# Optimization experiments

Measured on AMD Instinct MI355X. Metric: run time of the kernel, lower is better.

## Reference

```python
import jax, jax.numpy as jnp
import numpy as np

VOCAB = 128
NUM_PATHS = 100     # num_paths sampled from the lattice
NBEST_SCALE = 0.5   # scale on scores before sampling (k2.random_paths)
TEMPERATURE = 1.0   # logprob temperature before normalization
BLANK = 0           # CTC blank token


def setup_inputs() -> dict:
    key = jax.random.key(0)
    k1, k2, k3, k4 = jax.random.split(key, 4)
    B, T, L = 8, 500, 100
    logits = jax.random.normal(k1, (B, T, VOCAB), jnp.float32)
    emissions = jax.nn.log_softmax(logits, -1)  # acoustic-model log-probs (N, T, C)
    emissions_lengths = jax.random.randint(k2, (B,), 400, T + 1).astype(jnp.int32)
    labels = jax.random.randint(k3, (B, L), 1, VOCAB).astype(jnp.int32)
    labels_length = jax.random.randint(k4, (B,), 80, L + 1).astype(jnp.int32)
    return {"emissions": emissions, "emissions_lengths": emissions_lengths,
            "labels": labels, "labels_length": labels_length}


def _mwer(emissions, emissions_lengths, labels, labels_length):
    B, T, V = emissions.shape
    L = labels.shape[1]
    P = NUM_PATHS
    key = jax.random.key(1)
    # --- N-best path sampling: Gumbel perturbation of nbest_scale-scaled log-probs ---
    u = jax.random.uniform(key, (B, P, T, V), emissions.dtype, 1e-6, 1.0 - 1e-6)
    g = -jnp.log(-jnp.log(u))
    tokens = jnp.argmax(emissions[:, None] * NBEST_SCALE + g, axis=-1)  # (B, P, T)
    frame_mask = jnp.arange(T)[None, None, :] < emissions_lengths[:, None, None]
    # path log-prob under the model (unscaled scores), temperature-scaled
    lp = jnp.take_along_axis(emissions[:, None], tokens[..., None], axis=-1)[..., 0]
    path_logp = jnp.sum(jnp.where(frame_mask, lp, 0.0), axis=-1) / TEMPERATURE  # (B, P)
    # --- CTC collapse (ctc_topo semantics: drop blanks + repeats) into padded hyps ---
    prev = jnp.concatenate([jnp.full_like(tokens[..., :1], -1), tokens[..., :-1]], -1)
    keep = (tokens != BLANK) & (tokens != prev) & frame_mask
    pos = jnp.where(keep, jnp.cumsum(keep, -1) - 1, T)  # dropped frames -> dump slot T
    BP = B * P
    tok2, pos2 = tokens.reshape(BP, T), pos.reshape(BP, T)
    hyp = jnp.full((BP, T + 1), -1, tokens.dtype).at[jnp.arange(BP)[:, None], pos2].set(tok2)[:, :T]
    hyp_len = keep.reshape(BP, T).sum(-1)
    # --- Levenshtein alignment: exact edit distance hyp vs ref (vectorized DP) ---
    refs = jnp.repeat(labels, P, axis=0)             # (BP, L)  hyp_to_ref_map
    ref_len = jnp.repeat(labels_length, P, axis=0)   # (BP,)
    dp0 = jnp.broadcast_to(jnp.arange(L + 1, dtype=jnp.int32), (BP, L + 1))
    js = jnp.arange(L + 1, dtype=jnp.int32)[None, :]

    def step(dp, x):
        h, valid = x  # hyp token (BP,), valid flag (BP,)
        cost = (refs != h[:, None]).astype(jnp.int32)                       # (BP, L)
        cand = jnp.concatenate([dp[:, :1] + 1,
                                jnp.minimum(dp[:, 1:] + 1, dp[:, :-1] + cost)], 1)
        # insertion chain new[j] = min(cand[j], new[j-1]+1) via min-plus prefix
        new = jax.lax.cummin(cand - js, axis=1) + js
        return jnp.where(valid[:, None], new, dp), None

    valid = jnp.arange(T)[:, None] < hyp_len[None, :]  # (T, BP)
    dp, _ = jax.lax.scan(step, dp0, (hyp.T, valid))
    wers = jnp.take_along_axis(dp, ref_len[:, None], 1)[:, 0].reshape(B, P)
    wers = jax.lax.stop_gradient(wers.astype(emissions.dtype))
    # --- MWER: normalize path posteriors per utterance, expected WER, 'mean' ---
    prob = jax.nn.softmax(path_logp, axis=1)
    return jnp.mean(prob * wers)


def reference(emissions, emissions_lengths, labels, labels_length):
    return _mwer(emissions, emissions_lengths, labels, labels_length)
```

## Files before the change

kernel.cpp:

```cpp
#include <hip/hip_runtime.h>
#include <stdint.h>

#define NB 8
#define NP 100
#define NT 500
#define NV 128
#define NBP 800
#define TS 512
#define ES 500
#define PAIRS (NB * NT * 25)
#define NSB 1563

typedef unsigned long long u64;

#define ROTL(x, r) __builtin_amdgcn_alignbit((x), (x), 32 - (r))

#define SIDX(v) ((v) + ((v) >> 5))

__device__ __forceinline__ void threefry4_lo(uint32_t cA, uint32_t cB,
                                             uint32_t cC, uint32_t cD,
                                             uint32_t& oA, uint32_t& oB,
                                             uint32_t& oC, uint32_t& oD) {
  const uint32_t K2 = 0x1BD11BDBu;
  uint32_t a0 = 0u, a1 = cA + 1u;
  uint32_t b0 = 0u, b1 = cB + 1u;
  uint32_t c0 = 0u, c1 = cC + 1u;
  uint32_t d0 = 0u, d1 = cD + 1u;
#define PIN4() asm volatile("" : "+v"(a1), "+v"(b1), "+v"(c1), "+v"(d1))
#define R4(r) \
  a0 += a1; b0 += b1; c0 += c1; d0 += d1; \
  a1 = ROTL(a1, r) ^ a0; b1 = ROTL(b1, r) ^ b0; \
  c1 = ROTL(c1, r) ^ c0; d1 = ROTL(d1, r) ^ d0; \
  PIN4();
#define K4(kx, ky) \
  a0 += (kx); b0 += (kx); c0 += (kx); d0 += (kx); \
  a1 += (ky); b1 += (ky); c1 += (ky); d1 += (ky);
  R4(13) R4(15) R4(26) R4(6)
  K4(1u, K2 + 1u)
  R4(17) R4(29) R4(16) R4(24)
  K4(K2, 2u)
  R4(13) R4(15) R4(26) R4(6)
  K4(0u, 4u)
  R4(17) R4(29) R4(16) R4(24)
  K4(1u, K2 + 4u)
  R4(13) R4(15) R4(26) R4(6)
  oA = a1 + 5u; oB = b1 + 5u;
  oC = c1 + 5u; oD = d1 + 5u;
#undef R4
#undef K4
#undef PIN4
}

__global__ __launch_bounds__(256) void k_sample(
    const float* __restrict__ em, const int* __restrict__ elen,
    uint8_t* __restrict__ tok2, float* __restrict__ lp2t,
    const int* __restrict__ labels, const int* __restrict__ llen,
    uint4* __restrict__ pqg) {
  const int tid = threadIdx.x;
  if (blockIdx.x >= NSB) {
    const int b = blockIdx.x - NSB;
    if (tid < NV) {
      const int c = tid;
      const int m = llen[b];
      const int* __restrict__ lab = labels + b * 100;
      uint32_t a0 = 0, a1 = 0, a2 = 0, a3 = 0;
      const int e0 = m < 32 ? m : 32, e1 = m < 64 ? m : 64;
      const int e2 = m < 96 ? m : 96, e3 = m;
      for (int i = 0; i < e0; i++)  a0 |= (uint32_t)(lab[i] == c) << i;
      for (int i = 32; i < e1; i++) a1 |= (uint32_t)(lab[i] == c) << (i - 32);
      for (int i = 64; i < e2; i++) a2 |= (uint32_t)(lab[i] == c) << (i - 64);
      for (int i = 96; i < e3; i++) a3 |= (uint32_t)(lab[i] == c) << (i - 96);
      pqg[b * NV + c] = make_uint4(a0, a1, a2, a3);
    }
    return;
  }
  __shared__ float snw[4][NV + 4];
  const int pi0 = blockIdx.x * 64;
  const int R0 = pi0 / 25;
  for (int i = tid; i < 4 * NV; i += 256) {
    const int r = i >> 7, v = i & 127;
    int R = R0 + r; R = R < NB * NT ? R : NB * NT - 1;
    snw[r][SIDX(v)] = -__builtin_amdgcn_exp2f(em[(size_t)R * NV + v] * -0.7213475204444817f);
  }
  __syncthreads();
  const int gg = blockIdx.x * 256 + tid;
  const int pitem = gg >> 2, q = gg & 3;
  if (pitem >= PAIRS) return;
  const int R = pitem / 25;
  const int pp = pitem - R * 25;
  const int b = R / NT;
  const int t = R - b * NT;
  if (t >= elen[b]) return;
  const int r = R - R0;
  const int vh = q << 5;
  const int sbase = vh + q;
  const int bp0 = b * NP + 4 * pp;
  const uint32_t baseA = ((uint32_t)(bp0 * NT + t) << 7) + (uint32_t)vh;
  const uint32_t baseB = baseA + (uint32_t)(NT << 7);
  const uint32_t baseC = baseB + (uint32_t)(NT << 7);
  const uint32_t baseD = baseC + (uint32_t)(NT << 7);
  const float span = (float)(1.0 - 1e-6) - 1e-6f;
  float bvA = 3.0e38f, bvB = 3.0e38f, bvC = 3.0e38f, bvD = 3.0e38f;
  int biA = 0, biB = 0, biC = 0, biD = 0;
#pragma unroll 8
  for (int i = 0; i < 32; i++) {
    uint32_t rA, rB, rC, rD;
    threefry4_lo(baseA + (uint32_t)i, baseB + (uint32_t)i,
                 baseC + (uint32_t)i, baseD + (uint32_t)i, rA, rB, rC, rD);
    const float w = snw[r][sbase + i];
    const float fA = __uint_as_float((rA >> 9) | 0x3f800000u) - 1.0f;
    const float fB = __uint_as_float((rB >> 9) | 0x3f800000u) - 1.0f;
    const float fC = __uint_as_float((rC >> 9) | 0x3f800000u) - 1.0f;
    const float fD = __uint_as_float((rD >> 9) | 0x3f800000u) - 1.0f;
    const float uA = fmaf(fA, span, 1e-6f);
    const float uB = fmaf(fB, span, 1e-6f);
    const float uC = fmaf(fC, span, 1e-6f);
    const float uD = fmaf(fD, span, 1e-6f);
    const float sA = __log2f(uA) * w;
    const float sB = __log2f(uB) * w;
    const float sC = __log2f(uC) * w;
    const float sD = __log2f(uD) * w;
    if (sA < bvA) { bvA = sA; biA = vh + i; }
    if (sB < bvB) { bvB = sB; biB = vh + i; }
    if (sC < bvC) { bvC = sC; biC = vh + i; }
    if (sD < bvD) { bvD = sD; biD = vh + i; }
  }
#pragma unroll
  for (int off = 1; off <= 2; off <<= 1) {
    float ov; int oi;
    ov = __shfl_xor(bvA, off); oi = __shfl_xor(biA, off);
    if (ov < bvA || (ov == bvA && oi < biA)) { bvA = ov; biA = oi; }
    ov = __shfl_xor(bvB, off); oi = __shfl_xor(biB, off);
    if (ov < bvB || (ov == bvB && oi < biB)) { bvB = ov; biB = oi; }
    ov = __shfl_xor(bvC, off); oi = __shfl_xor(biC, off);
    if (ov < bvC || (ov == bvC && oi < biC)) { bvC = ov; biC = oi; }
    ov = __shfl_xor(bvD, off); oi = __shfl_xor(biD, off);
    if (ov < bvD || (ov == bvD && oi < biD)) { bvD = ov; biD = oi; }
  }
  if (q == 0) {
    const float* __restrict__ erow = em + (size_t)R * NV;
    const float eA = erow[biA], eB = erow[biB], eC = erow[biC], eD = erow[biD];
    tok2[(size_t)(bp0 + 0) * TS + t] = (uint8_t)biA;
    tok2[(size_t)(bp0 + 1) * TS + t] = (uint8_t)biB;
    tok2[(size_t)(bp0 + 2) * TS + t] = (uint8_t)biC;
    tok2[(size_t)(bp0 + 3) * TS + t] = (uint8_t)biD;
    *(float4*)&lp2t[(size_t)t * NBP + bp0] = make_float4(eA, eB, eC, eD);
  }
}

__global__ __launch_bounds__(64) void k_ce(
    const uint8_t* __restrict__ tok2, const uint4* __restrict__ pqg,
    const int* __restrict__ elen, uint4* __restrict__ eqc,
    int* __restrict__ nkept) {
  __shared__ uint4 pqs[NV];
  const int bp = blockIdx.x;
  const int b = bp / NP;
  const int lane = threadIdx.x;
  pqs[lane] = pqg[b * NV + lane];
  pqs[lane + 64] = pqg[b * NV + lane + 64];
  __syncthreads();
  const int el = elen[b];
  const uint8_t* __restrict__ row = tok2 + (size_t)bp * TS;
  uint4* __restrict__ orow = eqc + (size_t)bp * ES;
  int off = 0;
  for (int t0 = 0; t0 < el; t0 += 64) {
    const int t = t0 + lane;
    const bool inb = (t < el);
    const int c = inb ? row[t] : 0;
    const int cp = (t == 0) ? 255 : (inb ? row[t - 1] : 255);
    const bool kept = inb && (c != 0) && (c != cp);
    const u64 mask = __ballot(kept);
    const int idx = off + (int)__builtin_amdgcn_mbcnt_hi(
        (uint32_t)(mask >> 32),
        __builtin_amdgcn_mbcnt_lo((uint32_t)mask, 0u));
    if (kept) orow[idx] = pqs[c];
    off += (int)__popcll(mask);
  }
  if (lane == 0) nkept[bp] = off;
}

__device__ __forceinline__ void loadg(uint4 (&B)[4], int g, const uint4* __restrict__ rowp) {
#pragma unroll
  for (int i = 0; i < 4; i++) {
    int t = g * 4 + i;
    t = t < ES ? t : ES - 1;
    B[i] = rowp[t];
  }
}

__device__ __forceinline__ void procg(const uint4 (&B)[4], int fbase, int nk,
                                      u64 hmask,
                                      u64& Pv0, u64& Pv1, u64& Mv0, u64& Mv1,
                                      int& score) {
#pragma unroll
  for (int i = 0; i < 4; i++) {
    if (fbase + i >= nk) break;
    const u64 Eq0 = (u64)B[i].x | ((u64)B[i].y << 32);
    const u64 Eq1 = (u64)B[i].z | ((u64)B[i].w << 32);
    const u64 Xv0 = Eq0 | Mv0, Xv1 = Eq1 | Mv1;
    const u64 EP0 = Eq0 & Pv0, EP1 = Eq1 & Pv1;
    const u64 sA = EP0 + Pv0;
    const u64 sB = EP1 + Pv1 + (sA < EP0 ? 1ull : 0ull);
    const u64 Xh0 = (sA ^ Pv0) | Eq0;
    const u64 Xh1 = (sB ^ Pv1) | Eq1;
    const u64 Ph0 = Mv0 | ~(Xh0 | Pv0);
    const u64 Ph1 = Mv1 | ~(Xh1 | Pv1);
    const u64 Mh0 = Pv0 & Xh0, Mh1 = Pv1 & Xh1;
    score += (int)((Ph1 & hmask) != 0) - (int)((Mh1 & hmask) != 0);
    const u64 nPh1 = (Ph1 << 1) | (Ph0 >> 63);
    const u64 nPh0 = (Ph0 << 1) | 1ull;
    const u64 nMh1 = (Mh1 << 1) | (Mh0 >> 63);
    const u64 nMh0 = (Mh0 << 1);
    Pv0 = nMh0 | ~(Xv0 | nPh0);
    Pv1 = nMh1 | ~(Xv1 | nPh1);
    Mv0 = nPh0 & Xv0;
    Mv1 = nPh1 & Xv1;
  }
}

__global__ __launch_bounds__(128) void k_dpred(
    const uint4* __restrict__ eqc, const int* __restrict__ nkept,
    const int* __restrict__ llen, const float* __restrict__ lp2t,
    const int* __restrict__ elen, float* __restrict__ wer,
    double* __restrict__ pred) {
  const int blk = blockIdx.x;
  const int tid = threadIdx.x;
  if (blk >= 16) {
    const int i = blk - 16;
    const int b = i >> 2, k = i & 3;
    const bool active = (tid < NP);
    const int p = active ? tid : NP - 1;
    const int el = elen[b];
    const int t0 = k * 125;
    const int t1 = (t0 + 125 < el) ? t0 + 125 : el;
    const float* __restrict__ col = lp2t + b * NP + p;
    double s = 0.0;
#pragma unroll 8
    for (int t = t0; t < t1; t++) s += (double)col[(size_t)t * NBP];
    if (active) pred[(size_t)(b * NP + p) * 4 + k] = s;
    return;
  }
  if (tid >= 64) return;
  const int b = blk >> 1, h = blk & 1;
  const bool active = (tid < 50);
  const int bp = b * NP + h * 50 + (active ? tid : 49);
  const int m = llen[b];
  const int nk = nkept[bp];
  const uint4* __restrict__ rowp = eqc + (size_t)bp * ES;
  u64 Pv0 = ~0ull, Pv1 = ~0ull, Mv0 = 0ull, Mv1 = 0ull;
  int score = m;
  const u64 hmask = 1ull << ((m - 1) & 63);

  const int ngl = (nk + 3) >> 2;
  int ngmax = ngl;
  for (int off = 1; off < 64; off <<= 1) {
    const int o = __shfl_xor(ngmax, off);
    ngmax = o > ngmax ? o : ngmax;
  }
  uint4 B0[4], B1[4], B2[4], B3[4];
  loadg(B0, 0, rowp); loadg(B1, 1, rowp);
  loadg(B2, 2, rowp); loadg(B3, 3, rowp);
  int g = 0;
  while (g + 4 <= ngmax) {
    procg(B0, (g    ) * 4, nk, hmask, Pv0, Pv1, Mv0, Mv1, score);
    loadg(B0, g + 4, rowp);
    procg(B1, (g + 1) * 4, nk, hmask, Pv0, Pv1, Mv0, Mv1, score);
    loadg(B1, g + 5, rowp);
    procg(B2, (g + 2) * 4, nk, hmask, Pv0, Pv1, Mv0, Mv1, score);
    loadg(B2, g + 6, rowp);
    procg(B3, (g + 3) * 4, nk, hmask, Pv0, Pv1, Mv0, Mv1, score);
    loadg(B3, g + 7, rowp);
    g += 4;
  }
  if (g     < ngmax) procg(B0, (g    ) * 4, nk, hmask, Pv0, Pv1, Mv0, Mv1, score);
  if (g + 1 < ngmax) procg(B1, (g + 1) * 4, nk, hmask, Pv0, Pv1, Mv0, Mv1, score);
  if (g + 2 < ngmax) procg(B2, (g + 2) * 4, nk, hmask, Pv0, Pv1, Mv0, Mv1, score);
  if (active) wer[bp] = (float)score;
}

__global__ __launch_bounds__(512) void k_fin(
    const double* __restrict__ pred, const float* __restrict__ wer,
    float* __restrict__ out) {
  __shared__ float partial[NB];
  const int w = threadIdx.x >> 6, lane = threadIdx.x & 63;
  const int base = w * NP;
  float l0 = -1e30f, l1 = -1e30f;
  if (lane < NP) {
    const double* pr = pred + (size_t)(base + lane) * 4;
    l0 = (float)(pr[0] + pr[1] + pr[2] + pr[3]);
  }
  if (lane + 64 < NP) {
    const double* pr = pred + (size_t)(base + lane + 64) * 4;
    l1 = (float)(pr[0] + pr[1] + pr[2] + pr[3]);
  }
  float mx = fmaxf(l0, l1);
  for (int off = 1; off < 64; off <<= 1) mx = fmaxf(mx, __shfl_xor(mx, off));
  const float e0 = (lane < NP) ? __expf(l0 - mx) : 0.0f;
  const float e1 = (lane + 64 < NP) ? __expf(l1 - mx) : 0.0f;
  const float w0 = (lane < NP) ? wer[base + lane] : 0.0f;
  const float w1 = (lane + 64 < NP) ? wer[base + lane + 64] : 0.0f;
  float s = e0 + e1;
  float a = e0 * w0 + e1 * w1;
  for (int off = 1; off < 64; off <<= 1) {
    s += __shfl_xor(s, off);
    a += __shfl_xor(a, off);
  }
  if (lane == 0) partial[w] = a / s;
  __syncthreads();
  if (threadIdx.x == 0) {
    float tot = 0.0f;
    for (int i = 0; i < NB; i++) tot += partial[i];
    out[0] = tot * (1.0f / (float)NBP);
  }
}

extern "C" void kernel_launch(void* const* d_in, const int* in_sizes, int n_in,
                              void* d_out, int out_size, void* d_ws, size_t ws_size,
                              hipStream_t stream) {
  const float* em     = (const float*)d_in[0];
  const int*   elen   = (const int*)d_in[1];
  const int*   labels = (const int*)d_in[2];
  const int*   llen   = (const int*)d_in[3];
  float* out = (float*)d_out;
  char* ws = (char*)d_ws;
  uint4*   eqc   = (uint4*)ws;
  uint8_t* tok2  = (uint8_t*)(ws + 6400000);
  float*   lp2t  = (float*)(ws + 6809600);
  float*   wer   = (float*)(ws + 8409600);
  double*  pred  = (double*)(ws + 8412800);
  int*     nkept = (int*)(ws + 8438400);
  uint4*   pqg   = (uint4*)(ws + 8441600);

  k_sample<<<dim3(NSB + NB), dim3(256), 0, stream>>>(em, elen, tok2, lp2t,
                                                     labels, llen, pqg);
  k_ce<<<dim3(NBP), dim3(64), 0, stream>>>(tok2, pqg, elen, eqc, nkept);
  k_dpred<<<dim3(48), dim3(128), 0, stream>>>(eqc, nkept, llen, lp2t, elen, wer, pred);
  k_fin<<<dim3(1), dim3(512), 0, stream>>>(pred, wer, out);
}
```

Baseline: 189.3 us.

## Transpose Myers bit-parallel edit distance to iterate over reference labels

```diff
diff --git a/kernel.cpp b/kernel.cpp
--- a/kernel.cpp
+++ b/kernel.cpp
@@ -7,7 +7,6 @@
 #define NV 128
 #define NBP 800
 #define TS 512
-#define ES 500
 #define PAIRS (NB * NT * 25)
 #define NSB 1563
 
@@ -53,28 +52,9 @@
 
 __global__ __launch_bounds__(256) void k_sample(
     const float* __restrict__ em, const int* __restrict__ elen,
-    uint8_t* __restrict__ tok2, float* __restrict__ lp2t,
-    const int* __restrict__ labels, const int* __restrict__ llen,
-    uint4* __restrict__ pqg) {
+    uint8_t* __restrict__ tok2, float* __restrict__ lp2t) {
+  __shared__ float snw[4][NV + 4];
   const int tid = threadIdx.x;
-  if (blockIdx.x >= NSB) {
-    const int b = blockIdx.x - NSB;
-    if (tid < NV) {
-      const int c = tid;
-      const int m = llen[b];
-      const int* __restrict__ lab = labels + b * 100;
-      uint32_t a0 = 0, a1 = 0, a2 = 0, a3 = 0;
-      const int e0 = m < 32 ? m : 32, e1 = m < 64 ? m : 64;
-      const int e2 = m < 96 ? m : 96, e3 = m;
-      for (int i = 0; i < e0; i++)  a0 |= (uint32_t)(lab[i] == c) << i;
-      for (int i = 32; i < e1; i++) a1 |= (uint32_t)(lab[i] == c) << (i - 32);
-      for (int i = 64; i < e2; i++) a2 |= (uint32_t)(lab[i] == c) << (i - 64);
-      for (int i = 96; i < e3; i++) a3 |= (uint32_t)(lab[i] == c) << (i - 96);
-      pqg[b * NV + c] = make_uint4(a0, a1, a2, a3);
-    }
-    return;
-  }
-  __shared__ float snw[4][NV + 4];
   const int pi0 = blockIdx.x * 64;
   const int R0 = pi0 / 25;
   for (int i = tid; i < 4 * NV; i += 256) {
@@ -149,19 +129,14 @@
 }
 
 __global__ __launch_bounds__(64) void k_ce(
-    const uint8_t* __restrict__ tok2, const uint4* __restrict__ pqg,
-    const int* __restrict__ elen, uint4* __restrict__ eqc,
-    int* __restrict__ nkept) {
-  __shared__ uint4 pqs[NV];
+    const uint8_t* __restrict__ tok2, const int* __restrict__ elen,
+    uint8_t* __restrict__ chyp, int* __restrict__ nkept) {
   const int bp = blockIdx.x;
   const int b = bp / NP;
   const int lane = threadIdx.x;
-  pqs[lane] = pqg[b * NV + lane];
-  pqs[lane + 64] = pqg[b * NV + lane + 64];
-  __syncthreads();
   const int el = elen[b];
   const uint8_t* __restrict__ row = tok2 + (size_t)bp * TS;
-  uint4* __restrict__ orow = eqc + (size_t)bp * ES;
+  uint8_t* __restrict__ orow = chyp + (size_t)bp * TS;
   int off = 0;
   for (int t0 = 0; t0 < el; t0 += 64) {
     const int t = t0 + lane;
@@ -173,53 +148,48 @@
     const int idx = off + (int)__builtin_amdgcn_mbcnt_hi(
         (uint32_t)(mask >> 32),
         __builtin_amdgcn_mbcnt_lo((uint32_t)mask, 0u));
-    if (kept) orow[idx] = pqs[c];
+    if (kept) orow[idx] = (uint8_t)c;
     off += (int)__popcll(mask);
   }
+  for (int t = off + lane; t < TS; t += 64) orow[t] = 0;
   if (lane == 0) nkept[bp] = off;
 }
 
-__device__ __forceinline__ void loadg(uint4 (&B)[4], int g, const uint4* __restrict__ rowp) {
-#pragma unroll
-  for (int i = 0; i < 4; i++) {
-    int t = g * 4 + i;
-    t = t < ES ? t : ES - 1;
-    B[i] = rowp[t];
-  }
-}
-
-__device__ __forceinline__ void procg(const uint4 (&B)[4], int fbase, int nk,
-                                      u64 hmask,
-                                      u64& Pv0, u64& Pv1, u64& Mv0, u64& Mv1,
-                                      int& score) {
-#pragma unroll
-  for (int i = 0; i < 4; i++) {
-    if (fbase + i >= nk) break;
-    const u64 Eq0 = (u64)B[i].x | ((u64)B[i].y << 32);
-    const u64 Eq1 = (u64)B[i].z | ((u64)B[i].w << 32);
-    const u64 Xv0 = Eq0 | Mv0, Xv1 = Eq1 | Mv1;
-    const u64 EP0 = Eq0 & Pv0, EP1 = Eq1 & Pv1;
-    const u64 sA = EP0 + Pv0;
-    const u64 sB = EP1 + Pv1 + (sA < EP0 ? 1ull : 0ull);
-    const u64 Xh0 = (sA ^ Pv0) | Eq0;
-    const u64 Xh1 = (sB ^ Pv1) | Eq1;
-    const u64 Ph0 = Mv0 | ~(Xh0 | Pv0);
-    const u64 Ph1 = Mv1 | ~(Xh1 | Pv1);
-    const u64 Mh0 = Pv0 & Xh0, Mh1 = Pv1 & Xh1;
-    score += (int)((Ph1 & hmask) != 0) - (int)((Mh1 & hmask) != 0);
-    const u64 nPh1 = (Ph1 << 1) | (Ph0 >> 63);
-    const u64 nPh0 = (Ph0 << 1) | 1ull;
-    const u64 nMh1 = (Mh1 << 1) | (Mh0 >> 63);
-    const u64 nMh0 = (Mh0 << 1);
-    Pv0 = nMh0 | ~(Xv0 | nPh0);
-    Pv1 = nMh1 | ~(Xv1 | nPh1);
-    Mv0 = nPh0 & Xv0;
-    Mv1 = nPh1 & Xv1;
+__global__ __launch_bounds__(128) void k_col(
+    const uint8_t* __restrict__ chyp, const int* __restrict__ labels,
+    const int* __restrict__ llen, const int* __restrict__ elen,
+    u64* __restrict__ eqw) {
+  __shared__ uint32_t ch[TS / 4];
+  const int bp = blockIdx.x;
+  const int b = bp / NP;
+  const int j = threadIdx.x;
+  const uint32_t* __restrict__ src = (const uint32_t*)(chyp + (size_t)bp * TS);
+  ch[j] = src[j];
+  __syncthreads();
+  const int m = llen[b];
+  const int el = elen[b];
+  if (j >= m) return;
+  const uint32_t rj = (uint32_t)labels[b * 100 + j];
+  u64* __restrict__ dst = eqw + bp;
+#pragma unroll
+  for (int w = 0; w < 8; w++) {
+    u64 acc = 0;
+    const int i0 = w * 64;
+    if (i0 < el) {
+      for (int k = 0; k < 64; k += 4) {
+        const uint32_t wd = ch[(i0 + k) >> 2];
+        acc |= (u64)((wd & 255u) == rj) << k;
+        acc |= (u64)(((wd >> 8) & 255u) == rj) << (k + 1);
+        acc |= (u64)(((wd >> 16) & 255u) == rj) << (k + 2);
+        acc |= (u64)((wd >> 24) == rj) << (k + 3);
+      }
+    }
+    dst[(size_t)(j * 8 + w) * NBP] = acc;
   }
 }
 
 __global__ __launch_bounds__(128) void k_dpred(
-    const uint4* __restrict__ eqc, const int* __restrict__ nkept,
+    const u64* __restrict__ eqw, const int* __restrict__ nkept,
     const int* __restrict__ llen, const float* __restrict__ lp2t,
     const int* __restrict__ elen, float* __restrict__ wer,
     double* __restrict__ pred) {
@@ -246,35 +216,71 @@
   const int bp = b * NP + h * 50 + (active ? tid : 49);
   const int m = llen[b];
   const int nk = nkept[bp];
-  const uint4* __restrict__ rowp = eqc + (size_t)bp * ES;
-  u64 Pv0 = ~0ull, Pv1 = ~0ull, Mv0 = 0ull, Mv1 = 0ull;
-  int score = m;
-  const u64 hmask = 1ull << ((m - 1) & 63);
-
-  const int ngl = (nk + 3) >> 2;
-  int ngmax = ngl;
-  for (int off = 1; off < 64; off <<= 1) {
-    const int o = __shfl_xor(ngmax, off);
-    ngmax = o > ngmax ? o : ngmax;
-  }
-  uint4 B0[4], B1[4], B2[4], B3[4];
-  loadg(B0, 0, rowp); loadg(B1, 1, rowp);
-  loadg(B2, 2, rowp); loadg(B3, 3, rowp);
-  int g = 0;
-  while (g + 4 <= ngmax) {
-    procg(B0, (g    ) * 4, nk, hmask, Pv0, Pv1, Mv0, Mv1, score);
-    loadg(B0, g + 4, rowp);
-    procg(B1, (g + 1) * 4, nk, hmask, Pv0, Pv1, Mv0, Mv1, score);
-    loadg(B1, g + 5, rowp);
-    procg(B2, (g + 2) * 4, nk, hmask, Pv0, Pv1, Mv0, Mv1, score);
-    loadg(B2, g + 6, rowp);
-    procg(B3, (g + 3) * 4, nk, hmask, Pv0, Pv1, Mv0, Mv1, score);
-    loadg(B3, g + 7, rowp);
-    g += 4;
-  }
-  if (g     < ngmax) procg(B0, (g    ) * 4, nk, hmask, Pv0, Pv1, Mv0, Mv1, score);
-  if (g + 1 < ngmax) procg(B1, (g + 1) * 4, nk, hmask, Pv0, Pv1, Mv0, Mv1, score);
-  if (g + 2 < ngmax) procg(B2, (g + 2) * 4, nk, hmask, Pv0, Pv1, Mv0, Mv1, score);
+  const int nkc = nk < 1 ? 1 : nk;
+  const int wsel = (nkc - 1) >> 6;
+  const u64 hm = 1ull << ((nkc - 1) & 63);
+  const bool s1 = (wsel & 1) != 0, s2 = (wsel & 2) != 0, s4 = (wsel & 4) != 0;
+  u64 Pv[8], Mv[8];
+#pragma unroll
+  for (int w = 0; w < 8; w++) { Pv[w] = ~0ull; Mv[w] = 0ull; }
+  int score = nk;
+  const u64* __restrict__ base = eqw + bp;
+  u64 cur[8], nxt[8];
+#pragma unroll
+  for (int w = 0; w < 8; w++) cur[w] = base[(size_t)w * NBP];
+  for (int j = 0; j < m; j++) {
+    if (j + 1 < m) {
+      const u64* __restrict__ nb = base + (size_t)(j + 1) * 8 * NBP;
+#pragma unroll
+      for (int w = 0; w < 8; w++) nxt[w] = nb[(size_t)w * NBP];
+    }
+    u64 Xv[8], Ph[8], Mh[8];
+    u64 carry = 0;
+#pragma unroll
+    for (int w = 0; w < 8; w++) {
+      const u64 Eq = cur[w];
+      Xv[w] = Eq | Mv[w];
+      const u64 EP = Eq & Pv[w];
+      const u64 t1 = EP + Pv[w];
+      const u64 c1 = (u64)(t1 < EP);
+      const u64 s = t1 + carry;
+      const u64 c2 = (u64)(s < t1);
+      carry = c1 | c2;
+      const u64 Xh = (s ^ Pv[w]) | Eq;
+      Ph[w] = Mv[w] | ~(Xh | Pv[w]);
+      Mh[w] = Pv[w] & Xh;
+      Pv[w] = Xh;
+    }
+    const u64 p01 = s1 ? Ph[1] : Ph[0];
+    const u64 p23 = s1 ? Ph[3] : Ph[2];
+    const u64 p45 = s1 ? Ph[5] : Ph[4];
+    const u64 p67 = s1 ? Ph[7] : Ph[6];
+    const u64 m01 = s1 ? Mh[1] : Mh[0];
+    const u64 m23 = s1 ? Mh[3] : Mh[2];
+    const u64 m45 = s1 ? Mh[5] : Mh[4];
+    const u64 m67 = s1 ? Mh[7] : Mh[6];
+    const u64 p03 = s2 ? p23 : p01;
+    const u64 p47 = s2 ? p67 : p45;
+    const u64 m03 = s2 ? m23 : m01;
+    const u64 m47 = s2 ? m67 : m45;
+    const u64 ph = s4 ? p47 : p03;
+    const u64 mh = s4 ? m47 : m03;
+    score += (int)((ph & hm) != 0) - (int)((mh & hm) != 0);
+    u64 phc = 1ull, mhc = 0ull;
+#pragma unroll
+    for (int w = 0; w < 8; w++) {
+      const u64 Xh = Pv[w];
+      const u64 nPh = (Ph[w] << 1) | phc;
+      const u64 nMh = (Mh[w] << 1) | mhc;
+      phc = Ph[w] >> 63;
+      mhc = Mh[w] >> 63;
+      Pv[w] = nMh | ~(Xv[w] | nPh);
+      Mv[w] = nPh & Xv[w];
+      (void)Xh;
+    }
+#pragma unroll
+    for (int w = 0; w < 8; w++) cur[w] = nxt[w];
+  }
   if (active) wer[bp] = (float)score;
 }
 
@@ -323,17 +329,17 @@
   const int*   llen   = (const int*)d_in[3];
   float* out = (float*)d_out;
   char* ws = (char*)d_ws;
-  uint4*   eqc   = (uint4*)ws;
-  uint8_t* tok2  = (uint8_t*)(ws + 6400000);
-  float*   lp2t  = (float*)(ws + 6809600);
-  float*   wer   = (float*)(ws + 8409600);
-  double*  pred  = (double*)(ws + 8412800);
-  int*     nkept = (int*)(ws + 8438400);
-  uint4*   pqg   = (uint4*)(ws + 8441600);
-
-  k_sample<<<dim3(NSB + NB), dim3(256), 0, stream>>>(em, elen, tok2, lp2t,
-                                                     labels, llen, pqg);
-  k_ce<<<dim3(NBP), dim3(64), 0, stream>>>(tok2, pqg, elen, eqc, nkept);
-  k_dpred<<<dim3(48), dim3(128), 0, stream>>>(eqc, nkept, llen, lp2t, elen, wer, pred);
+  u64*     eqw   = (u64*)ws;
+  uint8_t* tok2  = (uint8_t*)(ws + 5120000);
+  uint8_t* chyp  = (uint8_t*)(ws + 5529600);
+  float*   lp2t  = (float*)(ws + 5939200);
+  float*   wer   = (float*)(ws + 7539200);
+  double*  pred  = (double*)(ws + 7542400);
+  int*     nkept = (int*)(ws + 7568000);
+
+  k_sample<<<dim3(NSB), dim3(256), 0, stream>>>(em, elen, tok2, lp2t);
+  k_ce<<<dim3(NBP), dim3(64), 0, stream>>>(tok2, elen, chyp, nkept);
+  k_col<<<dim3(NBP), dim3(128), 0, stream>>>(chyp, labels, llen, elen, eqw);
+  k_dpred<<<dim3(48), dim3(128), 0, stream>>>(eqw, nkept, llen, lp2t, elen, wer, pred);
   k_fin<<<dim3(1), dim3(512), 0, stream>>>(pred, wer, out);
 }
```

New measurement: 218.1 us. 15.2% more time.
